# Kernel tuning notes

Hardware: AMD Instinct MI355X
Metric: run time of the kernel (lower is better)

Reference implementation:

```python
import jax, jax.numpy as jnp
import numpy as np

N = 50000      # num_nodes
E = 800000     # num_edges (avg degree 16)
D = 128        # input_dim = hidden_dim = output_dim
L = 3          # num_layers
EPS = 1e-5     # BatchNorm eps


def setup_inputs() -> dict:
    key = jax.random.key(0)
    k_x, k_e, k_w, k_b = jax.random.split(key, 4)
    x = jax.random.normal(k_x, (N, D), dtype=jnp.float32)
    edge_index = jax.random.randint(k_e, (2, E), 0, N, dtype=jnp.int32)
    # Stacked per-layer params: GCN weight/bias + BatchNorm gamma/beta
    Ws = jax.random.normal(k_w, (L, D, D), dtype=jnp.float32) * (1.0 / np.sqrt(D))
    bs = jax.random.normal(k_b, (L, D), dtype=jnp.float32) * 0.01
    gammas = jnp.ones((L, D), dtype=jnp.float32)
    betas = jnp.zeros((L, D), dtype=jnp.float32)
    return {"x": x, "edge_index": edge_index, "Ws": Ws, "bs": bs,
            "gammas": gammas, "betas": betas}


def reference(x, edge_index, Ws, bs, gammas, betas):
    """CausalGNN forward: L x (GCNConv -> BN(train stats) -> ReLU[not last]) with residuals.
    Dropout p=0 (deterministic). GCNConv is PyG-style: add self-loops, symmetric
    D^{-1/2} (A+I) D^{-1/2} normalization, linear transform + bias."""
    src, dst = edge_index[0], edge_index[1]
    # degree including self-loop (+1), computed at aggregation index
    deg = jax.ops.segment_sum(jnp.ones((E,), jnp.float32), dst, num_segments=N) + 1.0
    dis = jax.lax.rsqrt(deg)                       # deg >= 1, safe
    norm = dis[src] * dis[dst]                      # [E] edge norm
    self_norm = dis * dis                           # [N] self-loop norm = 1/deg

    for i in range(L):
        h = x @ Ws[i]                               # [N, D]
        # scatter-add aggregation of normalized neighbor messages
        agg = jax.ops.segment_sum(h[src] * norm[:, None], dst, num_segments=N)
        agg = agg + self_norm[:, None] * h + bs[i]
        # BatchNorm1d (training mode: biased batch statistics over nodes)
        mean = jnp.mean(agg, axis=0)
        var = jnp.mean(jnp.square(agg - mean), axis=0)
        y = gammas[i] * (agg - mean) * jax.lax.rsqrt(var + EPS) + betas[i]
        if i < L - 1:
            y = jax.nn.relu(y)
        x = x + y if i > 0 else y                   # residual (dims match)
    return x
```

## Files before the change

### kernel.cpp

```cpp
#include <hip/hip_runtime.h>
#include <hip/hip_bf16.h>
#include <hip/hip_fp16.h>

#define N_ 50000
#define E_ 800000
#define D_ 128
#define L_ 3

typedef _Float16 half8 __attribute__((ext_vector_type(8)));
typedef float f32x4 __attribute__((ext_vector_type(4)));


__device__ inline float4 hcvt(uint2 u) {
    __half2 h0 = *(__half2*)&u.x;
    __half2 h1 = *(__half2*)&u.y;
    float2 f0 = __half22float2(h0);
    float2 f1 = __half22float2(h1);
    return make_float4(f0.x, f0.y, f1.x, f1.y);
}

__device__ inline unsigned pkh(float a, float b) {
    __half2 h = __floats2half2_rn(a, b);
    return *(unsigned*)&h;
}

__device__ inline unsigned short pkh1(float a) {
    _Float16 h = (_Float16)a;
    return *(unsigned short*)&h;
}


__global__ void k_count(const int* __restrict__ dst, int* __restrict__ deg,
                        int* __restrict__ offbuf) {
    int e = blockIdx.x * 256 + threadIdx.x;
    if (e < E_) offbuf[e] = atomicAdd(&deg[dst[e]], 1);
}

__global__ __launch_bounds__(1024) void k_scan1(const int* __restrict__ deg,
                                                int* __restrict__ linc,
                                                int* __restrict__ bsum,
                                                float* __restrict__ dis) {
    __shared__ int wsum[16];
    int t    = threadIdx.x;
    int lane = t & 63;
    int wid  = t >> 6;
    int i    = blockIdx.x * 1024 + t;
    int d    = (i < N_) ? deg[i] : 0;
    if (i < N_) dis[i] = rsqrtf((float)d + 1.0f);
    int v = d;
#pragma unroll
    for (int off = 1; off < 64; off <<= 1) {
        int u = __shfl_up(v, off);
        if (lane >= off) v += u;
    }
    if (lane == 63) wsum[wid] = v;
    __syncthreads();
    if (wid == 0) {
        int w = (lane < 16) ? wsum[lane] : 0;
#pragma unroll
        for (int off = 1; off < 16; off <<= 1) {
            int u = __shfl_up(w, off);
            if (lane >= off) w += u;
        }
        if (lane < 16) wsum[lane] = w;
    }
    __syncthreads();
    int woff = (wid > 0) ? wsum[wid - 1] : 0;
    v += woff;
    if (i < N_) linc[i] = v;
    if (t == 1023) bsum[blockIdx.x] = v;
}

__global__ void k_scan2(const int* __restrict__ bsum, int* __restrict__ boff) {
    int lane = threadIdx.x;
    int v = (lane < 49) ? bsum[lane] : 0;
#pragma unroll
    for (int off = 1; off < 64; off <<= 1) {
        int u = __shfl_up(v, off);
        if (lane >= off) v += u;
    }
    if (lane < 49) boff[lane] = v - bsum[lane];
}

__global__ __launch_bounds__(1024) void k_scan3(const int* __restrict__ linc,
                                                const int* __restrict__ boff,
                                                int* __restrict__ row_ptr) {
    int i = blockIdx.x * 1024 + threadIdx.x;
    if (i < N_) row_ptr[i + 1] = linc[i] + boff[blockIdx.x];
    if (i == 0) row_ptr[0] = 0;
}

__global__ void k_fill(const int* __restrict__ src, const int* __restrict__ dst,
                       const int* __restrict__ row_ptr, const int* __restrict__ offbuf,
                       int* __restrict__ csr_src) {
    int e = blockIdx.x * 256 + threadIdx.x;
    if (e < E_) {
        int d = dst[e];
        csr_src[row_ptr[d] + offbuf[e]] = src[e];
    }
}


__global__ __launch_bounds__(256) void k_prew(const float* __restrict__ Ws,
                                              unsigned short* __restrict__ Wb) {
    int l = blockIdx.x;
    const float* Wl = Ws + l * 16384;
    unsigned short* Wo = Wb + l * 16384;
    for (int i = threadIdx.x; i < 16384; i += 256) {
        int n = i >> 7, k = i & 127;
        Wo[n * 128 + k] = pkh1(Wl[k * 128 + n]);
    }
}


__global__ __launch_bounds__(256) void k_gemm(const float* __restrict__ Xin,
                                              const unsigned short* __restrict__ Wb,
                                              const float* __restrict__ dis,
                                              uint4* __restrict__ Hb,
                                              const float* __restrict__ st,
                                              const float* __restrict__ gamma,
                                              const float* __restrict__ beta,
                                              const float* __restrict__ res,
                                              float* __restrict__ xout) {
    __shared__ unsigned short wt[128 * 136];
    __shared__ unsigned short xb[64 * 136];
    __shared__ float sab[256];
    int t  = threadIdx.x;
    int r0 = blockIdx.x * 64;

    if (st) {
        if (t < 128) {
            float s = 0.f, s2 = 0.f;
#pragma unroll
            for (int k = 0; k < 8; ++k) {
                s  += st[k * 256 + t];
                s2 += st[k * 256 + 128 + t];
            }
            float mean = s * (1.0f / N_);
            float var  = s2 * (1.0f / N_) - mean * mean;
            float a = gamma[t] * rsqrtf(var + 1e-5f);
            sab[t]       = a;
            sab[128 + t] = beta[t] - mean * a;
        }
        __syncthreads();
    }

#pragma unroll
    for (int j = 0; j < 8; ++j) {
        int i = t + 256 * j;
        int row = i >> 4, c16 = i & 15;
        *(uint4*)&wt[row * 136 + c16 * 8] = ((const uint4*)Wb)[i];
    }
#pragma unroll
    for (int j = 0; j < 8; ++j) {
        int g   = t + 256 * j;
        int row = g >> 5;
        int c4  = (g & 31) * 4;
        int gr  = r0 + row;
        float4 v = make_float4(0.f, 0.f, 0.f, 0.f);
        if (gr < N_) {
            v = *(const float4*)(Xin + gr * 128 + c4);
            if (st) {
                v.x = fmaxf(sab[c4] * v.x + sab[128 + c4], 0.f);
                v.y = fmaxf(sab[c4 + 1] * v.y + sab[128 + c4 + 1], 0.f);
                v.z = fmaxf(sab[c4 + 2] * v.z + sab[128 + c4 + 2], 0.f);
                v.w = fmaxf(sab[c4 + 3] * v.w + sab[128 + c4 + 3], 0.f);
                if (res) {
                    float4 rr = *(const float4*)(res + gr * 128 + c4);
                    v.x += rr.x; v.y += rr.y; v.z += rr.z; v.w += rr.w;
                }
                *(float4*)(xout + gr * 128 + c4) = v;
            }
        }
        uint2 p;
        p.x = pkh(v.x, v.y);
        p.y = pkh(v.z, v.w);
        *(uint2*)&xb[row * 136 + c4] = p;
    }
    __syncthreads();

    int wv   = t >> 6;
    int lane = t & 63;
    int ln   = lane & 15;
    int quad = lane >> 4;

    const unsigned short* arow = &xb[(wv * 16 + ln) * 136 + quad * 8];
    half8 af[4];
#pragma unroll
    for (int ks = 0; ks < 4; ++ks) af[ks] = *(const half8*)(arow + ks * 32);

    f32x4 acc[8];
#pragma unroll
    for (int ct = 0; ct < 8; ++ct) acc[ct] = (f32x4){0.f, 0.f, 0.f, 0.f};

#pragma unroll
    for (int ct = 0; ct < 8; ++ct) {
        const unsigned short* wp = &wt[(ct * 16 + ln) * 136 + quad * 8];
#pragma unroll
        for (int ks = 0; ks < 4; ++ks) {
            half8 bf = *(const half8*)(wp + ks * 32);
            acc[ct] = __builtin_amdgcn_mfma_f32_16x16x32_f16(af[ks], bf, acc[ct], 0, 0, 0);
        }
    }

    float dr[4];
#pragma unroll
    for (int reg = 0; reg < 4; ++reg) {
        int r = r0 + wv * 16 + quad * 4 + reg;
        dr[reg] = dis[r < N_ ? r : (N_ - 1)];
    }
#pragma unroll
    for (int ct = 0; ct < 8; ++ct) {
#pragma unroll
        for (int reg = 0; reg < 4; ++reg) {
            int lrow = wv * 16 + quad * 4 + reg;
            xb[lrow * 136 + ct * 16 + ln] = pkh1(acc[ct][reg] * dr[reg]);
        }
    }
    __syncthreads();
#pragma unroll
    for (int j = 0; j < 4; ++j) {
        int i = t + 256 * j;
        int row = i >> 4, c16 = i & 15;
        int gr = r0 + row;
        if (gr < N_) Hb[gr * 16 + c16] = *(uint4*)&xb[row * 136 + c16 * 8];
    }
}


__global__ __launch_bounds__(256) void k_agg(const uint4* __restrict__ Hb,
                                             const int* __restrict__ row_ptr,
                                             const int* __restrict__ csr_src,
                                             const float* __restrict__ dis,
                                             const float* __restrict__ bias,
                                             float4* __restrict__ AGG,
                                             float* __restrict__ stats2) {
    int tid  = threadIdx.x;
    int sub  = tid >> 4;
    int lane = tid & 15;
    int node = blockIdx.x * 16 + sub;

    int beg = row_ptr[node], end = row_ptr[node + 1];
    uint4 su = Hb[node * 16 + lane];
    float4 acc0 = hcvt(make_uint2(su.x, su.y));
    float4 acc1 = hcvt(make_uint2(su.z, su.w));

    for (int c = beg; c < end; c += 16) {
        int m = end - c; if (m > 16) m = 16;
        int idx = (lane < m) ? csr_src[c + lane] : 0;
        int j = 0;
        for (; j + 4 <= m; j += 4) {
            int s0 = __shfl(idx, j, 16);
            int s1 = __shfl(idx, j + 1, 16);
            int s2 = __shfl(idx, j + 2, 16);
            int s3 = __shfl(idx, j + 3, 16);
            uint4 a0 = Hb[s0 * 16 + lane];
            uint4 a1 = Hb[s1 * 16 + lane];
            uint4 a2 = Hb[s2 * 16 + lane];
            uint4 a3 = Hb[s3 * 16 + lane];
            float4 f00 = hcvt(make_uint2(a0.x, a0.y)), f01 = hcvt(make_uint2(a0.z, a0.w));
            float4 f10 = hcvt(make_uint2(a1.x, a1.y)), f11 = hcvt(make_uint2(a1.z, a1.w));
            float4 f20 = hcvt(make_uint2(a2.x, a2.y)), f21 = hcvt(make_uint2(a2.z, a2.w));
            float4 f30 = hcvt(make_uint2(a3.x, a3.y)), f31 = hcvt(make_uint2(a3.z, a3.w));
            acc0.x += f00.x + f10.x + f20.x + f30.x;
            acc0.y += f00.y + f10.y + f20.y + f30.y;
            acc0.z += f00.z + f10.z + f20.z + f30.z;
            acc0.w += f00.w + f10.w + f20.w + f30.w;
            acc1.x += f01.x + f11.x + f21.x + f31.x;
            acc1.y += f01.y + f11.y + f21.y + f31.y;
            acc1.z += f01.z + f11.z + f21.z + f31.z;
            acc1.w += f01.w + f11.w + f21.w + f31.w;
        }
        for (; j < m; ++j) {
            int s0 = __shfl(idx, j, 16);
            uint4 a0 = Hb[s0 * 16 + lane];
            float4 f00 = hcvt(make_uint2(a0.x, a0.y)), f01 = hcvt(make_uint2(a0.z, a0.w));
            acc0.x += f00.x; acc0.y += f00.y; acc0.z += f00.z; acc0.w += f00.w;
            acc1.x += f01.x; acc1.y += f01.y; acc1.z += f01.z; acc1.w += f01.w;
        }
    }

    float dn = dis[node];
    float4 b0 = *(const float4*)(bias + lane * 8);
    float4 b1 = *(const float4*)(bias + lane * 8 + 4);
    float4 r0, r1;
    r0.x = dn * acc0.x + b0.x; r0.y = dn * acc0.y + b0.y;
    r0.z = dn * acc0.z + b0.z; r0.w = dn * acc0.w + b0.w;
    r1.x = dn * acc1.x + b1.x; r1.y = dn * acc1.y + b1.y;
    r1.z = dn * acc1.z + b1.z; r1.w = dn * acc1.w + b1.w;
    AGG[node * 32 + lane * 2]     = r0;
    AGG[node * 32 + lane * 2 + 1] = r1;

    __shared__ float sbuf[16][128];
    float4* sp = (float4*)&sbuf[sub][lane * 8];
    sp[0] = r0; sp[1] = r1;
    __syncthreads();
    if (tid < 128) {
        float s = 0.f, s2 = 0.f;
#pragma unroll
        for (int k = 0; k < 16; ++k) {
            float v = sbuf[k][tid];
            s += v; s2 += v * v;
        }
        float* stp = stats2 + (blockIdx.x & 7) * 256;
        atomicAdd(&stp[tid], s);
        atomicAdd(&stp[128 + tid], s2);
    }
}


__global__ __launch_bounds__(256) void k_normF(const float4* __restrict__ AGG,
                                               const float4* __restrict__ res,
                                               const float* __restrict__ st,
                                               const float* __restrict__ gamma,
                                               const float* __restrict__ beta,
                                               float4* __restrict__ OUT) {
    __shared__ float sab[256];
    int t = threadIdx.x;
    if (t < 128) {
        float s = 0.f, s2 = 0.f;
#pragma unroll
        for (int k = 0; k < 8; ++k) {
            s  += st[k * 256 + t];
            s2 += st[k * 256 + 128 + t];
        }
        float mean = s * (1.0f / N_);
        float var  = s2 * (1.0f / N_) - mean * mean;
        float a = gamma[t] * rsqrtf(var + 1e-5f);
        sab[t]       = a;
        sab[128 + t] = beta[t] - mean * a;
    }
    __syncthreads();
    for (int i = blockIdx.x * 256 + t; i < N_ * 32; i += gridDim.x * 256) {
        int f4 = (i & 31) * 4;
        float4 v = AGG[i];
        float4 rr = res[i];
        v.x = sab[f4] * v.x + sab[128 + f4] + rr.x;
        v.y = sab[f4 + 1] * v.y + sab[128 + f4 + 1] + rr.y;
        v.z = sab[f4 + 2] * v.z + sab[128 + f4 + 2] + rr.z;
        v.w = sab[f4 + 3] * v.w + sab[128 + f4 + 3] + rr.w;
        OUT[i] = v;
    }
}


extern "C" void kernel_launch(void* const* d_in, const int* in_sizes, int n_in,
                              void* d_out, int out_size, void* d_ws, size_t ws_size,
                              hipStream_t stream) {
    const float* x      = (const float*)d_in[0];
    const int*   ei     = (const int*)d_in[1];
    const float* Ws     = (const float*)d_in[2];
    const float* bs     = (const float*)d_in[3];
    const float* gammas = (const float*)d_in[4];
    const float* betas  = (const float*)d_in[5];
    float* out = (float*)d_out;

    const int* src = ei;
    const int* dst = ei + E_;

    char* w = (char*)d_ws;
    int*   deg     = (int*)(w + 0);
    float* stats2  = (float*)(w + 200000);
    int*   row_ptr = (int*)(w + 224576);
    float* dis     = (float*)(w + 424592);
    int*   offbuf  = (int*)(w + 624592);
    int*   csr_src = (int*)(w + 3824592);
    uint4* Hb      = (uint4*)(w + 7024640);
    float* XB      = (float*)(w + 19824640);
    unsigned short* Wb = (unsigned short*)offbuf;
    float* AGG     = out;

    int* linc = (int*)XB;
    int* bsum = (int*)XB + N_;
    int* boff = (int*)XB + N_ + 64;

    hipMemsetAsync(d_ws, 0, 224576, stream);

    k_count<<<(E_ + 255) / 256, 256, 0, stream>>>(dst, deg, offbuf);
    k_scan1<<<49, 1024, 0, stream>>>(deg, linc, bsum, dis);
    k_scan2<<<1, 64, 0, stream>>>(bsum, boff);
    k_scan3<<<49, 1024, 0, stream>>>(linc, boff, row_ptr);
    k_fill<<<(E_ + 255) / 256, 256, 0, stream>>>(src, dst, row_ptr, offbuf, csr_src);
    k_prew<<<3, 256, 0, stream>>>(Ws, Wb);

    const int GG = (N_ + 63) / 64;
    k_gemm<<<GG, 256, 0, stream>>>(x, Wb, dis, Hb,
                                   nullptr, nullptr, nullptr, nullptr, nullptr);
    k_agg<<<N_ / 16, 256, 0, stream>>>(Hb, row_ptr, csr_src, dis, bs,
                                       (float4*)AGG, stats2);
    k_gemm<<<GG, 256, 0, stream>>>(AGG, Wb + 16384, dis, Hb,
                                   stats2, gammas, betas, nullptr, XB);
    k_agg<<<N_ / 16, 256, 0, stream>>>(Hb, row_ptr, csr_src, dis, bs + D_,
                                       (float4*)AGG, stats2 + 2048);
    k_gemm<<<GG, 256, 0, stream>>>(AGG, Wb + 32768, dis, Hb,
                                   stats2 + 2048, gammas + D_, betas + D_, XB, XB);
    k_agg<<<N_ / 16, 256, 0, stream>>>(Hb, row_ptr, csr_src, dis, bs + 2 * D_,
                                       (float4*)AGG, stats2 + 4096);
    k_normF<<<512, 256, 0, stream>>>((const float4*)AGG, (const float4*)XB,
                                     stats2 + 4096, gammas + 2 * D_, betas + 2 * D_,
                                     (float4*)out);
}
```

Baseline: 312.7 us.

## Split fp16 feature matrix into four column panels and aggregate panel by panel

The GEMM now writes its fp16 output as four separate column panels of 32 features (64 bytes per node) instead of one 256-byte row per node. The aggregation kernel is restructured as a persistent grid of 625 blocks that sweeps each panel in turn over several node groups. This shrinks the working set per pass so gathered neighbour rows are more likely to stay in cache. The cost is 64-byte scattered gathers with less data per request, four passes over the CSR indices, and a different BatchNorm stats reduction through shared memory.

```diff
diff --git a/kernel.cpp b/kernel.cpp
--- a/kernel.cpp
+++ b/kernel.cpp
@@ -7,17 +7,12 @@
 #define D_ 128
 #define L_ 3
 
+#define AGG_BLOCKS 625
+#define AGG_GPB 5
+
 typedef _Float16 half8 __attribute__((ext_vector_type(8)));
 typedef float f32x4 __attribute__((ext_vector_type(4)));
 
-
-__device__ inline float4 hcvt(uint2 u) {
-    __half2 h0 = *(__half2*)&u.x;
-    __half2 h1 = *(__half2*)&u.y;
-    float2 f0 = __half22float2(h0);
-    float2 f1 = __half22float2(h1);
-    return make_float4(f0.x, f0.y, f1.x, f1.y);
-}
 
 __device__ inline unsigned pkh(float a, float b) {
     __half2 h = __floats2half2_rn(a, b);
@@ -27,6 +22,10 @@
 __device__ inline unsigned short pkh1(float a) {
     _Float16 h = (_Float16)a;
     return *(unsigned short*)&h;
+}
+
+__device__ inline float2 h2f2(unsigned u) {
+    return __half22float2(*(__half2*)&u);
 }
 
 
@@ -116,7 +115,7 @@
 __global__ __launch_bounds__(256) void k_gemm(const float* __restrict__ Xin,
                                               const unsigned short* __restrict__ Wb,
                                               const float* __restrict__ dis,
-                                              uint4* __restrict__ Hb,
+                                              uint4* __restrict__ Hb4,
                                               const float* __restrict__ st,
                                               const float* __restrict__ gamma,
                                               const float* __restrict__ beta,
@@ -209,6 +208,7 @@
         int r = r0 + wv * 16 + quad * 4 + reg;
         dr[reg] = dis[r < N_ ? r : (N_ - 1)];
     }
+    __syncthreads();
 #pragma unroll
     for (int ct = 0; ct < 8; ++ct) {
 #pragma unroll
@@ -220,91 +220,93 @@
     __syncthreads();
 #pragma unroll
     for (int j = 0; j < 4; ++j) {
-        int i = t + 256 * j;
-        int row = i >> 4, c16 = i & 15;
-        int gr = r0 + row;
-        if (gr < N_) Hb[gr * 16 + c16] = *(uint4*)&xb[row * 136 + c16 * 8];
-    }
-}
-
-
-__global__ __launch_bounds__(256) void k_agg(const uint4* __restrict__ Hb,
+        int n_local = t >> 2;
+        int q = t & 3;
+        int gr = r0 + n_local;
+        if (gr < N_)
+            Hb4[j * (N_ * 4) + gr * 4 + q] = *(uint4*)&xb[n_local * 136 + j * 32 + q * 8];
+    }
+}
+
+
+__global__ __launch_bounds__(256) void k_agg(const unsigned* __restrict__ Hu,
                                              const int* __restrict__ row_ptr,
                                              const int* __restrict__ csr_src,
                                              const float* __restrict__ dis,
                                              const float* __restrict__ bias,
-                                             float4* __restrict__ AGG,
+                                             float2* __restrict__ AGG,
                                              float* __restrict__ stats2) {
     int tid  = threadIdx.x;
     int sub  = tid >> 4;
     int lane = tid & 15;
-    int node = blockIdx.x * 16 + sub;
-
-    int beg = row_ptr[node], end = row_ptr[node + 1];
-    uint4 su = Hb[node * 16 + lane];
-    float4 acc0 = hcvt(make_uint2(su.x, su.y));
-    float4 acc1 = hcvt(make_uint2(su.z, su.w));
-
-    for (int c = beg; c < end; c += 16) {
-        int m = end - c; if (m > 16) m = 16;
-        int idx = (lane < m) ? csr_src[c + lane] : 0;
-        int j = 0;
-        for (; j + 4 <= m; j += 4) {
-            int s0 = __shfl(idx, j, 16);
-            int s1 = __shfl(idx, j + 1, 16);
-            int s2 = __shfl(idx, j + 2, 16);
-            int s3 = __shfl(idx, j + 3, 16);
-            uint4 a0 = Hb[s0 * 16 + lane];
-            uint4 a1 = Hb[s1 * 16 + lane];
-            uint4 a2 = Hb[s2 * 16 + lane];
-            uint4 a3 = Hb[s3 * 16 + lane];
-            float4 f00 = hcvt(make_uint2(a0.x, a0.y)), f01 = hcvt(make_uint2(a0.z, a0.w));
-            float4 f10 = hcvt(make_uint2(a1.x, a1.y)), f11 = hcvt(make_uint2(a1.z, a1.w));
-            float4 f20 = hcvt(make_uint2(a2.x, a2.y)), f21 = hcvt(make_uint2(a2.z, a2.w));
-            float4 f30 = hcvt(make_uint2(a3.x, a3.y)), f31 = hcvt(make_uint2(a3.z, a3.w));
-            acc0.x += f00.x + f10.x + f20.x + f30.x;
-            acc0.y += f00.y + f10.y + f20.y + f30.y;
-            acc0.z += f00.z + f10.z + f20.z + f30.z;
-            acc0.w += f00.w + f10.w + f20.w + f30.w;
-            acc1.x += f01.x + f11.x + f21.x + f31.x;
-            acc1.y += f01.y + f11.y + f21.y + f31.y;
-            acc1.z += f01.z + f11.z + f21.z + f31.z;
-            acc1.w += f01.w + f11.w + f21.w + f31.w;
-        }
-        for (; j < m; ++j) {
-            int s0 = __shfl(idx, j, 16);
-            uint4 a0 = Hb[s0 * 16 + lane];
-            float4 f00 = hcvt(make_uint2(a0.x, a0.y)), f01 = hcvt(make_uint2(a0.z, a0.w));
-            acc0.x += f00.x; acc0.y += f00.y; acc0.z += f00.z; acc0.w += f00.w;
-            acc1.x += f01.x; acc1.y += f01.y; acc1.z += f01.z; acc1.w += f01.w;
-        }
-    }
-
-    float dn = dis[node];
-    float4 b0 = *(const float4*)(bias + lane * 8);
-    float4 b1 = *(const float4*)(bias + lane * 8 + 4);
-    float4 r0, r1;
-    r0.x = dn * acc0.x + b0.x; r0.y = dn * acc0.y + b0.y;
-    r0.z = dn * acc0.z + b0.z; r0.w = dn * acc0.w + b0.w;
-    r1.x = dn * acc1.x + b1.x; r1.y = dn * acc1.y + b1.y;
-    r1.z = dn * acc1.z + b1.z; r1.w = dn * acc1.w + b1.w;
-    AGG[node * 32 + lane * 2]     = r0;
-    AGG[node * 32 + lane * 2 + 1] = r1;
-
-    __shared__ float sbuf[16][128];
-    float4* sp = (float4*)&sbuf[sub][lane * 8];
-    sp[0] = r0; sp[1] = r1;
-    __syncthreads();
-    if (tid < 128) {
-        float s = 0.f, s2 = 0.f;
-#pragma unroll
-        for (int k = 0; k < 16; ++k) {
-            float v = sbuf[k][tid];
-            s += v; s2 += v * v;
-        }
-        float* stp = stats2 + (blockIdx.x & 7) * 256;
-        atomicAdd(&stp[tid], s);
-        atomicAdd(&stp[128 + tid], s2);
+
+    float st_[4][4];
+#pragma unroll
+    for (int p = 0; p < 4; ++p)
+#pragma unroll
+        for (int i = 0; i < 4; ++i) st_[p][i] = 0.f;
+
+#pragma unroll
+    for (int p = 0; p < 4; ++p) {
+        const unsigned* Hp = Hu + p * (N_ * 16);
+        for (int gi = 0; gi < AGG_GPB; ++gi) {
+            int g    = gi * AGG_BLOCKS + blockIdx.x;
+            int node = g * 16 + sub;
+            int beg = row_ptr[node], end = row_ptr[node + 1];
+            float2 acc = h2f2(Hp[node * 16 + lane]);
+
+            for (int c = beg; c < end; c += 16) {
+                int m = end - c; if (m > 16) m = 16;
+                int idx = (lane < m) ? csr_src[c + lane] : 0;
+                int j = 0;
+                for (; j + 4 <= m; j += 4) {
+                    int s0 = __shfl(idx, j, 16);
+                    int s1 = __shfl(idx, j + 1, 16);
+                    int s2 = __shfl(idx, j + 2, 16);
+                    int s3 = __shfl(idx, j + 3, 16);
+                    unsigned u0 = Hp[s0 * 16 + lane];
+                    unsigned u1 = Hp[s1 * 16 + lane];
+                    unsigned u2 = Hp[s2 * 16 + lane];
+                    unsigned u3 = Hp[s3 * 16 + lane];
+                    float2 f0 = h2f2(u0), f1 = h2f2(u1), f2 = h2f2(u2), f3 = h2f2(u3);
+                    acc.x += f0.x + f1.x + f2.x + f3.x;
+                    acc.y += f0.y + f1.y + f2.y + f3.y;
+                }
+                for (; j < m; ++j) {
+                    int s0 = __shfl(idx, j, 16);
+                    float2 f0 = h2f2(Hp[s0 * 16 + lane]);
+                    acc.x += f0.x; acc.y += f0.y;
+                }
+            }
+
+            float dn = dis[node];
+            int f0 = p * 32 + lane * 2;
+            float2 b2 = *(const float2*)(bias + f0);
+            float2 r;
+            r.x = dn * acc.x + b2.x;
+            r.y = dn * acc.y + b2.y;
+            AGG[node * 64 + p * 16 + lane] = r;
+            st_[p][0] += r.x; st_[p][1] += r.x * r.x;
+            st_[p][2] += r.y; st_[p][3] += r.y * r.y;
+        }
+    }
+
+    __shared__ float red[16][64];
+    float* stp = stats2 + (blockIdx.x & 7) * 256;
+#pragma unroll
+    for (int p = 0; p < 4; ++p) {
+        *(float4*)&red[sub][lane * 4] =
+            make_float4(st_[p][0], st_[p][1], st_[p][2], st_[p][3]);
+        __syncthreads();
+        if (tid < 64) {
+            int lane2 = tid >> 2, slot = tid & 3;
+            float s = 0.f;
+#pragma unroll
+            for (int k = 0; k < 16; ++k) s += red[k][tid];
+            int f = p * 32 + lane2 * 2 + (slot >> 1);
+            atomicAdd(&stp[(slot & 1) * 128 + f], s);
+        }
+        __syncthreads();
     }
 }
 
@@ -365,7 +367,7 @@
     float* dis     = (float*)(w + 424592);
     int*   offbuf  = (int*)(w + 624592);
     int*   csr_src = (int*)(w + 3824592);
-    uint4* Hb      = (uint4*)(w + 7024640);
+    uint4* Hb4     = (uint4*)(w + 7024640);
     float* XB      = (float*)(w + 19824640);
     unsigned short* Wb = (unsigned short*)offbuf;
     float* AGG     = out;
@@ -384,18 +386,18 @@
     k_prew<<<3, 256, 0, stream>>>(Ws, Wb);
 
     const int GG = (N_ + 63) / 64;
-    k_gemm<<<GG, 256, 0, stream>>>(x, Wb, dis, Hb,
+    k_gemm<<<GG, 256, 0, stream>>>(x, Wb, dis, Hb4,
                                    nullptr, nullptr, nullptr, nullptr, nullptr);
-    k_agg<<<N_ / 16, 256, 0, stream>>>(Hb, row_ptr, csr_src, dis, bs,
-                                       (float4*)AGG, stats2);
-    k_gemm<<<GG, 256, 0, stream>>>(AGG, Wb + 16384, dis, Hb,
+    k_agg<<<AGG_BLOCKS, 256, 0, stream>>>((const unsigned*)Hb4, row_ptr, csr_src, dis,
+                                          bs, (float2*)AGG, stats2);
+    k_gemm<<<GG, 256, 0, stream>>>(AGG, Wb + 16384, dis, Hb4,
                                    stats2, gammas, betas, nullptr, XB);
-    k_agg<<<N_ / 16, 256, 0, stream>>>(Hb, row_ptr, csr_src, dis, bs + D_,
-                                       (float4*)AGG, stats2 + 2048);
-    k_gemm<<<GG, 256, 0, stream>>>(AGG, Wb + 32768, dis, Hb,
+    k_agg<<<AGG_BLOCKS, 256, 0, stream>>>((const unsigned*)Hb4, row_ptr, csr_src, dis,
+                                          bs + D_, (float2*)AGG, stats2 + 2048);
+    k_gemm<<<GG, 256, 0, stream>>>(AGG, Wb + 32768, dis, Hb4,
                                    stats2 + 2048, gammas + D_, betas + D_, XB, XB);
-    k_agg<<<N_ / 16, 256, 0, stream>>>(Hb, row_ptr, csr_src, dis, bs + 2 * D_,
-                                       (float4*)AGG, stats2 + 4096);
+    k_agg<<<AGG_BLOCKS, 256, 0, stream>>>((const unsigned*)Hb4, row_ptr, csr_src, dis,
+                                          bs + 2 * D_, (float2*)AGG, stats2 + 4096);
     k_normF<<<512, 256, 0, stream>>>((const float4*)AGG, (const float4*)XB,
                                      stats2 + 4096, gammas + 2 * D_, betas + 2 * D_,
                                      (float4*)out);
```

After: 505.4 us. 61.7% more time.

## Sort nodes by degree via counting sort to balance aggregation work

Applied to the files above, without the earlier changes.

Adds a degree histogram, a scan and an ordering pass that bucket nodes by in-degree (capped at 63), and makes the aggregation kernel process nodes in this degree-sorted order. Nodes grouped in a block then have similar edge counts, which reduces load imbalance and divergence across the 16 subgroups of each block. In exchange it adds three small kernels, an indirection load per node, and scattered writes of AGG rows that lose locality. A __syncthreads is also added in the GEMM epilogue before staging into shared memory, which looks like a correctness fix for a shared-buffer hazard.

```diff
diff --git a/kernel.cpp b/kernel.cpp
--- a/kernel.cpp
+++ b/kernel.cpp
@@ -34,6 +34,37 @@
                         int* __restrict__ offbuf) {
     int e = blockIdx.x * 256 + threadIdx.x;
     if (e < E_) offbuf[e] = atomicAdd(&deg[dst[e]], 1);
+}
+
+__global__ void k_hist(const int* __restrict__ deg, int* __restrict__ hist) {
+    __shared__ int lh[64];
+    if (threadIdx.x < 64) lh[threadIdx.x] = 0;
+    __syncthreads();
+    int i = blockIdx.x * 256 + threadIdx.x;
+    if (i < N_) atomicAdd(&lh[min(deg[i], 63)], 1);
+    __syncthreads();
+    if (threadIdx.x < 64 && lh[threadIdx.x]) atomicAdd(&hist[threadIdx.x], lh[threadIdx.x]);
+}
+
+__global__ void k_hscan(const int* __restrict__ hist, int* __restrict__ hoff) {
+    int lane = threadIdx.x;
+    int v = hist[lane];
+    int s = v;
+#pragma unroll
+    for (int off = 1; off < 64; off <<= 1) {
+        int u = __shfl_up(s, off);
+        if (lane >= off) s += u;
+    }
+    hoff[lane] = s - v;
+}
+
+__global__ void k_order(const int* __restrict__ deg, int* __restrict__ hoff,
+                        int* __restrict__ order) {
+    int i = blockIdx.x * 256 + threadIdx.x;
+    if (i < N_) {
+        int pos = atomicAdd(&hoff[min(deg[i], 63)], 1);
+        order[pos] = i;
+    }
 }
 
 __global__ __launch_bounds__(1024) void k_scan1(const int* __restrict__ deg,
@@ -209,6 +240,7 @@
         int r = r0 + wv * 16 + quad * 4 + reg;
         dr[reg] = dis[r < N_ ? r : (N_ - 1)];
     }
+    __syncthreads();
 #pragma unroll
     for (int ct = 0; ct < 8; ++ct) {
 #pragma unroll
@@ -231,6 +263,7 @@
 __global__ __launch_bounds__(256) void k_agg(const uint4* __restrict__ Hb,
                                              const int* __restrict__ row_ptr,
                                              const int* __restrict__ csr_src,
+                                             const int* __restrict__ order,
                                              const float* __restrict__ dis,
                                              const float* __restrict__ bias,
                                              float4* __restrict__ AGG,
@@ -238,7 +271,7 @@
     int tid  = threadIdx.x;
     int sub  = tid >> 4;
     int lane = tid & 15;
-    int node = blockIdx.x * 16 + sub;
+    int node = order[blockIdx.x * 16 + sub];
 
     int beg = row_ptr[node], end = row_ptr[node + 1];
     uint4 su = Hb[node * 16 + lane];
@@ -361,12 +394,15 @@
     char* w = (char*)d_ws;
     int*   deg     = (int*)(w + 0);
     float* stats2  = (float*)(w + 200000);
-    int*   row_ptr = (int*)(w + 224576);
-    float* dis     = (float*)(w + 424592);
-    int*   offbuf  = (int*)(w + 624592);
-    int*   csr_src = (int*)(w + 3824592);
-    uint4* Hb      = (uint4*)(w + 7024640);
-    float* XB      = (float*)(w + 19824640);
+    int*   hist    = (int*)(w + 224576);
+    int*   hoff    = (int*)(w + 224832);
+    int*   row_ptr = (int*)(w + 225088);
+    float* dis     = (float*)(w + 425092);
+    int*   offbuf  = (int*)(w + 625104);
+    int*   csr_src = (int*)(w + 3825104);
+    uint4* Hb      = (uint4*)(w + 7025104);
+    float* XB      = (float*)(w + 19825104);
+    int*   order   = (int*)(w + 45425104);
     unsigned short* Wb = (unsigned short*)offbuf;
     float* AGG     = out;
 
@@ -374,9 +410,12 @@
     int* bsum = (int*)XB + N_;
     int* boff = (int*)XB + N_ + 64;
 
-    hipMemsetAsync(d_ws, 0, 224576, stream);
+    hipMemsetAsync(d_ws, 0, 225088, stream);
 
     k_count<<<(E_ + 255) / 256, 256, 0, stream>>>(dst, deg, offbuf);
+    k_hist <<<(N_ + 255) / 256, 256, 0, stream>>>(deg, hist);
+    k_hscan<<<1, 64, 0, stream>>>(hist, hoff);
+    k_order<<<(N_ + 255) / 256, 256, 0, stream>>>(deg, hoff, order);
     k_scan1<<<49, 1024, 0, stream>>>(deg, linc, bsum, dis);
     k_scan2<<<1, 64, 0, stream>>>(bsum, boff);
     k_scan3<<<49, 1024, 0, stream>>>(linc, boff, row_ptr);
@@ -386,15 +425,15 @@
     const int GG = (N_ + 63) / 64;
     k_gemm<<<GG, 256, 0, stream>>>(x, Wb, dis, Hb,
                                    nullptr, nullptr, nullptr, nullptr, nullptr);
-    k_agg<<<N_ / 16, 256, 0, stream>>>(Hb, row_ptr, csr_src, dis, bs,
+    k_agg<<<N_ / 16, 256, 0, stream>>>(Hb, row_ptr, csr_src, order, dis, bs,
                                        (float4*)AGG, stats2);
     k_gemm<<<GG, 256, 0, stream>>>(AGG, Wb + 16384, dis, Hb,
                                    stats2, gammas, betas, nullptr, XB);
-    k_agg<<<N_ / 16, 256, 0, stream>>>(Hb, row_ptr, csr_src, dis, bs + D_,
+    k_agg<<<N_ / 16, 256, 0, stream>>>(Hb, row_ptr, csr_src, order, dis, bs + D_,
                                        (float4*)AGG, stats2 + 2048);
     k_gemm<<<GG, 256, 0, stream>>>(AGG, Wb + 32768, dis, Hb,
                                    stats2 + 2048, gammas + D_, betas + D_, XB, XB);
-    k_agg<<<N_ / 16, 256, 0, stream>>>(Hb, row_ptr, csr_src, dis, bs + 2 * D_,
+    k_agg<<<N_ / 16, 256, 0, stream>>>(Hb, row_ptr, csr_src, order, dis, bs + 2 * D_,
                                        (float4*)AGG, stats2 + 4096);
     k_normF<<<512, 256, 0, stream>>>((const float4*)AGG, (const float4*)XB,
                                      stats2 + 4096, gammas + 2 * D_, betas + 2 * D_,
```

Result: slower. 451.6 us (+44.4%).

## Store residual stream in fp16, fold scan2 into scan3, widen final norm grid

Applied to the files above, without the earlier changes.

The residual/skip tensor XB is now written and read as fp16 instead of fp32, which halves its traffic in the layer-2/3 GEMM prologue and in the final normalisation. The separate single-wave k_scan2 launch is removed. Each k_scan3 block now recomputes the prefix over the block sums itself, saving one kernel launch. The final k_normF grid doubles to 1024 blocks, and a __syncthreads is added before the GEMM epilogue reuses the xb shared buffer. The cost is fp16 rounding of the residual path, which reduces accuracy.

```diff
diff --git a/kernel.cpp b/kernel.cpp
--- a/kernel.cpp
+++ b/kernel.cpp
@@ -71,22 +71,24 @@
     if (t == 1023) bsum[blockIdx.x] = v;
 }
 
-__global__ void k_scan2(const int* __restrict__ bsum, int* __restrict__ boff) {
-    int lane = threadIdx.x;
-    int v = (lane < 49) ? bsum[lane] : 0;
-#pragma unroll
-    for (int off = 1; off < 64; off <<= 1) {
-        int u = __shfl_up(v, off);
-        if (lane >= off) v += u;
-    }
-    if (lane < 49) boff[lane] = v - bsum[lane];
-}
-
 __global__ __launch_bounds__(1024) void k_scan3(const int* __restrict__ linc,
-                                                const int* __restrict__ boff,
+                                                const int* __restrict__ bsum,
                                                 int* __restrict__ row_ptr) {
-    int i = blockIdx.x * 1024 + threadIdx.x;
-    if (i < N_) row_ptr[i + 1] = linc[i] + boff[blockIdx.x];
+    __shared__ int sboff;
+    int t = threadIdx.x;
+    if (t < 64) {
+        int v = (t < 49) ? bsum[t] : 0;
+#pragma unroll
+        for (int off = 1; off < 64; off <<= 1) {
+            int u = __shfl_up(v, off);
+            if (t >= off) v += u;
+        }
+        int ex = (blockIdx.x == 0) ? 0 : __shfl(v, (int)blockIdx.x - 1, 64);
+        if (t == 0) sboff = ex;
+    }
+    __syncthreads();
+    int i = blockIdx.x * 1024 + t;
+    if (i < N_) row_ptr[i + 1] = linc[i] + sboff;
     if (i == 0) row_ptr[0] = 0;
 }
 
@@ -120,8 +122,8 @@
                                               const float* __restrict__ st,
                                               const float* __restrict__ gamma,
                                               const float* __restrict__ beta,
-                                              const float* __restrict__ res,
-                                              float* __restrict__ xout) {
+                                              const unsigned short* __restrict__ resH,
+                                              unsigned short* __restrict__ xoutH) {
     __shared__ unsigned short wt[128 * 136];
     __shared__ unsigned short xb[64 * 136];
     __shared__ float sab[256];
@@ -165,16 +167,16 @@
                 v.y = fmaxf(sab[c4 + 1] * v.y + sab[128 + c4 + 1], 0.f);
                 v.z = fmaxf(sab[c4 + 2] * v.z + sab[128 + c4 + 2], 0.f);
                 v.w = fmaxf(sab[c4 + 3] * v.w + sab[128 + c4 + 3], 0.f);
-                if (res) {
-                    float4 rr = *(const float4*)(res + gr * 128 + c4);
+                if (resH) {
+                    float4 rr = hcvt(*(const uint2*)(resH + gr * 128 + c4));
                     v.x += rr.x; v.y += rr.y; v.z += rr.z; v.w += rr.w;
                 }
-                *(float4*)(xout + gr * 128 + c4) = v;
             }
         }
         uint2 p;
         p.x = pkh(v.x, v.y);
         p.y = pkh(v.z, v.w);
+        if (st && gr < N_) *(uint2*)(xoutH + gr * 128 + c4) = p;
         *(uint2*)&xb[row * 136 + c4] = p;
     }
     __syncthreads();
@@ -209,6 +211,7 @@
         int r = r0 + wv * 16 + quad * 4 + reg;
         dr[reg] = dis[r < N_ ? r : (N_ - 1)];
     }
+    __syncthreads();
 #pragma unroll
     for (int ct = 0; ct < 8; ++ct) {
 #pragma unroll
@@ -310,7 +313,7 @@
 
 
 __global__ __launch_bounds__(256) void k_normF(const float4* __restrict__ AGG,
-                                               const float4* __restrict__ res,
+                                               const unsigned short* __restrict__ resH,
                                                const float* __restrict__ st,
                                                const float* __restrict__ gamma,
                                                const float* __restrict__ beta,
@@ -334,7 +337,7 @@
     for (int i = blockIdx.x * 256 + t; i < N_ * 32; i += gridDim.x * 256) {
         int f4 = (i & 31) * 4;
         float4 v = AGG[i];
-        float4 rr = res[i];
+        float4 rr = hcvt(((const uint2*)resH)[i]);
         v.x = sab[f4] * v.x + sab[128 + f4] + rr.x;
         v.y = sab[f4 + 1] * v.y + sab[128 + f4 + 1] + rr.y;
         v.z = sab[f4 + 2] * v.z + sab[128 + f4 + 2] + rr.z;
@@ -366,20 +369,18 @@
     int*   offbuf  = (int*)(w + 624592);
     int*   csr_src = (int*)(w + 3824592);
     uint4* Hb      = (uint4*)(w + 7024640);
-    float* XB      = (float*)(w + 19824640);
-    unsigned short* Wb = (unsigned short*)offbuf;
+    unsigned short* XBh = (unsigned short*)(w + 19824640);
+    unsigned short* Wb  = (unsigned short*)offbuf;
     float* AGG     = out;
 
-    int* linc = (int*)XB;
-    int* bsum = (int*)XB + N_;
-    int* boff = (int*)XB + N_ + 64;
+    int* linc = (int*)XBh;
+    int* bsum = (int*)XBh + N_;
 
     hipMemsetAsync(d_ws, 0, 224576, stream);
 
     k_count<<<(E_ + 255) / 256, 256, 0, stream>>>(dst, deg, offbuf);
     k_scan1<<<49, 1024, 0, stream>>>(deg, linc, bsum, dis);
-    k_scan2<<<1, 64, 0, stream>>>(bsum, boff);
-    k_scan3<<<49, 1024, 0, stream>>>(linc, boff, row_ptr);
+    k_scan3<<<49, 1024, 0, stream>>>(linc, bsum, row_ptr);
     k_fill<<<(E_ + 255) / 256, 256, 0, stream>>>(src, dst, row_ptr, offbuf, csr_src);
     k_prew<<<3, 256, 0, stream>>>(Ws, Wb);
 
@@ -389,14 +390,14 @@
     k_agg<<<N_ / 16, 256, 0, stream>>>(Hb, row_ptr, csr_src, dis, bs,
                                        (float4*)AGG, stats2);
     k_gemm<<<GG, 256, 0, stream>>>(AGG, Wb + 16384, dis, Hb,
-                                   stats2, gammas, betas, nullptr, XB);
+                                   stats2, gammas, betas, nullptr, XBh);
     k_agg<<<N_ / 16, 256, 0, stream>>>(Hb, row_ptr, csr_src, dis, bs + D_,
                                        (float4*)AGG, stats2 + 2048);
     k_gemm<<<GG, 256, 0, stream>>>(AGG, Wb + 32768, dis, Hb,
-                                   stats2 + 2048, gammas + D_, betas + D_, XB, XB);
+                                   stats2 + 2048, gammas + D_, betas + D_, XBh, XBh);
     k_agg<<<N_ / 16, 256, 0, stream>>>(Hb, row_ptr, csr_src, dis, bs + 2 * D_,
                                        (float4*)AGG, stats2 + 4096);
-    k_normF<<<512, 256, 0, stream>>>((const float4*)AGG, (const float4*)XB,
-                                     stats2 + 4096, gammas + 2 * D_, betas + 2 * D_,
-                                     (float4*)out);
-}
+    k_normF<<<1024, 256, 0, stream>>>((const float4*)AGG, XBh,
+                                      stats2 + 4096, gammas + 2 * D_, betas + 2 * D_,
+                                      (float4*)out);
+}
```

Measured after the change: 303.6 us. 2.9% less time.
